# Kernel tuning notes

Hardware: AMD Instinct MI355X
Metric: run time of the kernel (lower is better)

## Reference

```python
import jax, jax.numpy as jnp
import numpy as np

B, F, H, C = 256, 512, 1024, 1000
LN_EPS = 1e-5


def _proj(x, W, b, g, be):
    # AdaptiveAvgPool2d(1) + Flatten + Linear + LayerNorm + GELU(exact)
    p = x.mean(axis=(2, 3))                       # [B, Cin]
    h = p @ W + b                                 # [B, F]
    mu = h.mean(axis=-1, keepdims=True)
    var = h.var(axis=-1, keepdims=True)           # ddof=0, matches torch LayerNorm
    h = (h - mu) / jnp.sqrt(var + LN_EPS) * g + be
    return jax.nn.gelu(h, approximate=False)


def setup_inputs() -> dict:
    key = jax.random.key(0)
    ks = iter(jax.random.split(key, 64))
    def rn(shape, s=1.0):
        return jax.random.normal(next(ks), shape, jnp.float32) * s
    inp = {}
    feats = {"s1": (16, 112), "s2": (24, 56), "s3": (40, 28), "s4": (80, 14), "s5": (160, 7)}
    for n, (c, hw) in feats.items():
        inp[n] = rn((B, c, hw, hw))
    inp["ff"] = rn((B, 960, 7, 7))
    for i, c in enumerate([16, 24, 40, 80, 160], start=1):
        inp[f"Wp{i}"] = rn((c, F), 0.02)
        inp[f"bp{i}"] = jnp.zeros((F,), jnp.float32)
        inp[f"g{i}"] = jnp.ones((F,), jnp.float32)
        inp[f"be{i}"] = jnp.zeros((F,), jnp.float32)
    inp["Wg1"] = rn((960, H), 0.02); inp["bg1"] = jnp.zeros((H,), jnp.float32)
    inp["Wg2"] = rn((H, H // 2), 0.02); inp["bg2"] = jnp.zeros((H // 2,), jnp.float32)
    inp["Wg3"] = rn((H // 2, 5), 0.02); inp["bg3"] = jnp.zeros((5,), jnp.float32)
    inp["Wc1"] = rn((F, H), 0.02); inp["bc1"] = jnp.zeros((H,), jnp.float32)
    inp["Wc2"] = rn((H, H // 2), 0.02); inp["bc2"] = jnp.zeros((H // 2,), jnp.float32)
    inp["Wc3"] = rn((H // 2, C), 0.02); inp["bc3"] = jnp.zeros((C,), jnp.float32)
    return inp


def reference(s1, s2, s3, s4, s5, ff,
              Wp1, bp1, g1, be1, Wp2, bp2, g2, be2, Wp3, bp3, g3, be3,
              Wp4, bp4, g4, be4, Wp5, bp5, g5, be5,
              Wg1, bg1, Wg2, bg2, Wg3, bg3,
              Wc1, bc1, Wc2, bc2, Wc3, bc3):
    # gate on pooled final backbone features (dropout inactive at eval)
    gate_in = ff.mean(axis=(2, 3))                         # [B, 960]
    h = jax.nn.relu(gate_in @ Wg1 + bg1)
    h = jax.nn.relu(h @ Wg2 + bg2)
    gate_logits = h @ Wg3 + bg3                            # [B, 5]

    # per-stage projections -> [B, 5, F]
    stack = jnp.stack([
        _proj(s1, Wp1, bp1, g1, be1),
        _proj(s2, Wp2, bp2, g2, be2),
        _proj(s3, Wp3, bp3, g3, be3),
        _proj(s4, Wp4, bp4, g4, be4),
        _proj(s5, Wp5, bp5, g5, be5),
    ], axis=1)

    topv, topi = jax.lax.top_k(gate_logits, 2)             # [B, 2]
    w = jax.nn.softmax(topv, axis=1)                       # softmax over top-k logits
    sel = jnp.take_along_axis(stack, topi[:, :, None], axis=1)  # [B, 2, F]
    mixture = (sel * w[:, :, None]).sum(axis=1)            # [B, F]

    h = jax.nn.relu(mixture @ Wc1 + bc1)
    h = jax.nn.relu(h @ Wc2 + bc2)
    logits = h @ Wc3 + bc3                                 # [B, C]
    return logits, gate_logits, topi, w
```

## Files before the change

kernel.cpp:

```cpp
#include <hip/hip_runtime.h>
#include <math.h>


struct PoolAll {
    const float* src[4];
    float*       dst[4];
    int n4[4];
    int cum[4];
    float inv[4];
    const float* s5;
    const float* ff;
    float*       dst5;
    float*       dstf;
    int nbb;
    int rows5;
};

__global__ __launch_bounds__(256) void pool_all_kernel(PoolAll S) {
    __shared__ float lds[64 * 49];
    if ((int)blockIdx.x < S.nbb) {
        int gid  = blockIdx.x * 256 + threadIdx.x;
        int wave = gid >> 6;
        int lane = gid & 63;
        if (wave >= S.cum[3]) return;
        int s = 0;
        #pragma unroll
        for (int i = 0; i < 3; ++i) if (wave >= S.cum[i]) s = i + 1;
        int row = wave - (s == 0 ? 0 : S.cum[s - 1]);
        const int n4 = S.n4[s];
        const float4* p4 = (const float4*)(S.src[s]) + (size_t)row * n4;
        float a0 = 0.f, a1 = 0.f, a2 = 0.f, a3 = 0.f;
        float a4 = 0.f, a5 = 0.f, a6 = 0.f, a7 = 0.f;
        int k = lane;
        for (; k + 448 < n4; k += 512) {
            float4 v0 = p4[k];       float4 v1 = p4[k + 64];
            float4 v2 = p4[k + 128]; float4 v3 = p4[k + 192];
            float4 v4 = p4[k + 256]; float4 v5 = p4[k + 320];
            float4 v6 = p4[k + 384]; float4 v7 = p4[k + 448];
            a0 += (v0.x + v0.y) + (v0.z + v0.w);
            a1 += (v1.x + v1.y) + (v1.z + v1.w);
            a2 += (v2.x + v2.y) + (v2.z + v2.w);
            a3 += (v3.x + v3.y) + (v3.z + v3.w);
            a4 += (v4.x + v4.y) + (v4.z + v4.w);
            a5 += (v5.x + v5.y) + (v5.z + v5.w);
            a6 += (v6.x + v6.y) + (v6.z + v6.w);
            a7 += (v7.x + v7.y) + (v7.z + v7.w);
        }
        for (; k + 192 < n4; k += 256) {
            float4 v0 = p4[k];       float4 v1 = p4[k + 64];
            float4 v2 = p4[k + 128]; float4 v3 = p4[k + 192];
            a0 += (v0.x + v0.y) + (v0.z + v0.w);
            a1 += (v1.x + v1.y) + (v1.z + v1.w);
            a2 += (v2.x + v2.y) + (v2.z + v2.w);
            a3 += (v3.x + v3.y) + (v3.z + v3.w);
        }
        for (; k < n4; k += 64) {
            float4 v = p4[k];
            a0 += (v.x + v.y) + (v.z + v.w);
        }
        float acc = ((a0 + a1) + (a2 + a3)) + ((a4 + a5) + (a6 + a7));
        #pragma unroll
        for (int off = 32; off > 0; off >>= 1) acc += __shfl_down(acc, off, 64);
        if (lane == 0) S.dst[s][row] = acc * S.inv[s];
        return;
    }
    const int tid  = threadIdx.x;
    const int row0 = (blockIdx.x - S.nbb) * 64;
    const float* src;
    float* dst;
    int rbase;
    if (row0 < S.rows5) { src = S.s5; dst = S.dst5; rbase = row0; }
    else                { src = S.ff; dst = S.dstf; rbase = row0 - S.rows5; }
    const float4* p4 = (const float4*)(src + (size_t)rbase * 49);
    float4* l4 = (float4*)lds;
    float4 v0 = p4[tid];
    float4 v1 = p4[tid + 256];
    float4 v2 = p4[tid + 512];
    float4 v3;
    const bool t3 = (tid < 784 - 768);
    if (t3) v3 = p4[tid + 768];
    l4[tid]       = v0;
    l4[tid + 256] = v1;
    l4[tid + 512] = v2;
    if (t3) l4[tid + 768] = v3;
    __syncthreads();
    const int r  = tid >> 2;
    const int c0 = tid & 3;
    float s = 0.f;
    #pragma unroll
    for (int c = c0; c < 49; c += 4) s += lds[r * 49 + c];
    s += __shfl_down(s, 2, 64);
    s += __shfl_down(s, 1, 64);
    if (c0 == 0) dst[rbase + r] = s * (1.f / 49.f);
}

template <int XKS, bool EPIB>
__global__ __launch_bounds__(256) void fc_tile_kernel(const float* __restrict__ X,
        const float* __restrict__ xbias, const float* __restrict__ W,
        float* __restrict__ P, const float* __restrict__ bias,
        int M, int K, int N, int Kc, int ntiles) {
    __shared__ __align__(16) float Xs[16][68];
    __shared__ __align__(16) float Ws[16][68];
    const int tpk = 4 * ntiles;
    int bid = blockIdx.x;
    int ks  = bid / tpk;
    int rem = bid - ks * tpk;
    int mt  = rem / ntiles;
    int nt  = rem - mt * ntiles;
    const int m0 = mt * 64, n0 = nt * 64;
    const int k0 = ks * Kc;
    int k1 = k0 + Kc; if (k1 > K) k1 = K;

    const int tid = threadIdx.x;
    const int tm = tid & 15;
    const int tn = tid >> 4;
    const int xr = tid >> 2, xc = tid & 3;
    const int wr = tid >> 4, wc = tid & 15;
    const int nwc = n0 + wc * 4;
    const size_t MK = (size_t)M * K;
    const size_t xoff0 = (size_t)(m0 + xr) * K;

    float4 acc[4];
    #pragma unroll
    for (int r = 0; r < 4; ++r) acc[r] = make_float4(0.f, 0.f, 0.f, 0.f);

    const int NXV = (XKS > 0) ? XKS : 1;
    float4 xv[NXV];
    float4 wv;

    {
        const size_t xo = xoff0 + k0 + xc * 4;
        #pragma unroll
        for (int ss = 0; ss < NXV; ++ss)
            xv[ss] = *(const float4*)(X + (size_t)ss * MK + xo);
        if (nwc + 3 < N) {
            wv = *(const float4*)(W + (size_t)(k0 + wr) * N + nwc);
        } else {
            wv.x = (nwc + 0 < N) ? W[(size_t)(k0 + wr) * N + nwc + 0] : 0.f;
            wv.y = (nwc + 1 < N) ? W[(size_t)(k0 + wr) * N + nwc + 1] : 0.f;
            wv.z = (nwc + 2 < N) ? W[(size_t)(k0 + wr) * N + nwc + 2] : 0.f;
            wv.w = (nwc + 3 < N) ? W[(size_t)(k0 + wr) * N + nwc + 3] : 0.f;
        }
    }

    for (int kt = k0; kt < k1; kt += 16) {
        __syncthreads();
        float4 xs = xv[0];
        if (XKS > 0) {
            #pragma unroll
            for (int ss = 1; ss < NXV; ++ss) {
                xs.x += xv[ss].x; xs.y += xv[ss].y;
                xs.z += xv[ss].z; xs.w += xv[ss].w;
            }
            float4 xb = *(const float4*)(xbias + kt + xc * 4);
            xs.x = fmaxf(xs.x + xb.x, 0.f);
            xs.y = fmaxf(xs.y + xb.y, 0.f);
            xs.z = fmaxf(xs.z + xb.z, 0.f);
            xs.w = fmaxf(xs.w + xb.w, 0.f);
        }
        Xs[xc * 4 + 0][xr] = xs.x;
        Xs[xc * 4 + 1][xr] = xs.y;
        Xs[xc * 4 + 2][xr] = xs.z;
        Xs[xc * 4 + 3][xr] = xs.w;
        *(float4*)&Ws[wr][wc * 4] = wv;
        __syncthreads();
        if (kt + 16 < k1) {
            const size_t xo = xoff0 + kt + 16 + xc * 4;
            #pragma unroll
            for (int ss = 0; ss < NXV; ++ss)
                xv[ss] = *(const float4*)(X + (size_t)ss * MK + xo);
            if (nwc + 3 < N) {
                wv = *(const float4*)(W + (size_t)(kt + 16 + wr) * N + nwc);
            } else {
                wv.x = (nwc + 0 < N) ? W[(size_t)(kt + 16 + wr) * N + nwc + 0] : 0.f;
                wv.y = (nwc + 1 < N) ? W[(size_t)(kt + 16 + wr) * N + nwc + 1] : 0.f;
                wv.z = (nwc + 2 < N) ? W[(size_t)(kt + 16 + wr) * N + nwc + 2] : 0.f;
                wv.w = (nwc + 3 < N) ? W[(size_t)(kt + 16 + wr) * N + nwc + 3] : 0.f;
            }
        }
        #pragma unroll
        for (int kk = 0; kk < 16; ++kk) {
            float4 xr4 = *(const float4*)&Xs[kk][tm * 4];
            float4 wr4 = *(const float4*)&Ws[kk][tn * 4];
            acc[0].x += xr4.x * wr4.x; acc[0].y += xr4.x * wr4.y;
            acc[0].z += xr4.x * wr4.z; acc[0].w += xr4.x * wr4.w;
            acc[1].x += xr4.y * wr4.x; acc[1].y += xr4.y * wr4.y;
            acc[1].z += xr4.y * wr4.z; acc[1].w += xr4.y * wr4.w;
            acc[2].x += xr4.z * wr4.x; acc[2].y += xr4.z * wr4.y;
            acc[2].z += xr4.z * wr4.z; acc[2].w += xr4.z * wr4.w;
            acc[3].x += xr4.w * wr4.x; acc[3].y += xr4.w * wr4.y;
            acc[3].z += xr4.w * wr4.z; acc[3].w += xr4.w * wr4.w;
        }
    }
    const int nbase = n0 + tn * 4;
    #pragma unroll
    for (int r = 0; r < 4; ++r) {
        int row = m0 + tm * 4 + r;
        float* pp = P + ((size_t)ks * M + row) * N + nbase;
        float4 v = acc[r];
        if (EPIB && nbase + 3 < N) {
            float4 bb = *(const float4*)(bias + nbase);
            v.x += bb.x; v.y += bb.y; v.z += bb.z; v.w += bb.w;
        }
        if (nbase + 3 < N) {
            *(float4*)pp = v;
        } else {
            float vv[4] = { v.x, v.y, v.z, v.w };
            for (int c = 0; c < 4; ++c)
                if (nbase + c < N) pp[c] = vv[c] + (EPIB ? bias[nbase + c] : 0.f);
        }
    }
}

struct ProjParams {
    const float* W[5];
    const float* bp[5];
    const float* g[5];
    const float* be[5];
    int K[5];
    int poff[5];
};

__global__ __launch_bounds__(256) void proj_gemm_kernel(ProjParams P,
        const float* __restrict__ pools, float* __restrict__ proj_out) {
    __shared__ __align__(16) float Xs[8][68];
    __shared__ __align__(16) float Ws[8][68];
    const int st = blockIdx.y;
    const int K  = P.K[st];
    const float* X = pools + P.poff[st];
    const float* W = P.W[st];
    const int N = 512;
    int bid = blockIdx.x;
    int mt  = bid >> 3;
    int nt  = bid & 7;
    const int m0 = mt * 64, n0 = nt * 64;

    const int tid = threadIdx.x;
    const int tm = tid & 15;
    const int tn = tid >> 4;
    const int xa = tid >> 3, xb = tid & 7;
    const int wc = tid & 63, wb = tid >> 6;
    const int nw = n0 + wc;

    float4 acc[4];
    #pragma unroll
    for (int r = 0; r < 4; ++r) acc[r] = make_float4(0.f, 0.f, 0.f, 0.f);

    float x0, x1, w0v, w1v;
    x0  = X[(size_t)(m0 + xa) * K + xb];
    x1  = X[(size_t)(m0 + xa + 32) * K + xb];
    w0v = W[(size_t)wb * N + nw];
    w1v = W[(size_t)(wb + 4) * N + nw];

    for (int kt = 0; kt < K; kt += 8) {
        __syncthreads();
        Xs[xb][xa] = x0; Xs[xb][xa + 32] = x1;
        Ws[wb][wc] = w0v; Ws[wb + 4][wc] = w1v;
        __syncthreads();
        if (kt + 8 < K) {
            x0  = X[(size_t)(m0 + xa) * K + kt + 8 + xb];
            x1  = X[(size_t)(m0 + xa + 32) * K + kt + 8 + xb];
            w0v = W[(size_t)(kt + 8 + wb) * N + nw];
            w1v = W[(size_t)(kt + 8 + wb + 4) * N + nw];
        }
        #pragma unroll
        for (int kk = 0; kk < 8; ++kk) {
            float4 xr = *(const float4*)&Xs[kk][tm * 4];
            float4 wr = *(const float4*)&Ws[kk][tn * 4];
            acc[0].x += xr.x * wr.x; acc[0].y += xr.x * wr.y;
            acc[0].z += xr.x * wr.z; acc[0].w += xr.x * wr.w;
            acc[1].x += xr.y * wr.x; acc[1].y += xr.y * wr.y;
            acc[1].z += xr.y * wr.z; acc[1].w += xr.y * wr.w;
            acc[2].x += xr.z * wr.x; acc[2].y += xr.z * wr.y;
            acc[2].z += xr.z * wr.z; acc[2].w += xr.z * wr.w;
            acc[3].x += xr.w * wr.x; acc[3].y += xr.w * wr.y;
            acc[3].z += xr.w * wr.z; acc[3].w += xr.w * wr.w;
        }
    }
    const int nbase = n0 + tn * 4;
    float4 bb = *(const float4*)(P.bp[st] + nbase);
    float* op = proj_out + (size_t)st * 131072 + (size_t)(m0 + tm * 4) * N + nbase;
    #pragma unroll
    for (int r = 0; r < 4; ++r) {
        float4 v = acc[r];
        v.x += bb.x; v.y += bb.y; v.z += bb.z; v.w += bb.w;
        *(float4*)(op + (size_t)r * N) = v;
    }
}

__global__ __launch_bounds__(256) void fc3_top2_kernel(const float* __restrict__ Xp,
        const float* __restrict__ xbias, const float* __restrict__ W,
        const float* __restrict__ bias, int* __restrict__ topi,
        float* __restrict__ wsm, float* __restrict__ out_gl,
        float* __restrict__ out_topi, float* __restrict__ out_w, int K) {
    const int b    = blockIdx.x;
    const int tid  = threadIdx.x;
    const int lane = tid & 63;
    const int wv   = tid >> 6;
    __shared__ float red[4][5];
    const size_t MK = (size_t)256 * K;
    float acc[5] = {0.f, 0.f, 0.f, 0.f, 0.f};
    for (int k = tid; k < K; k += 256) {
        float v = 0.f;
        #pragma unroll
        for (int s = 0; s < 16; ++s) v += Xp[(size_t)s * MK + (size_t)b * K + k];
        float xv = fmaxf(v + xbias[k], 0.f);
        const float* wr = W + (size_t)k * 5;
        acc[0] += xv * wr[0]; acc[1] += xv * wr[1]; acc[2] += xv * wr[2];
        acc[3] += xv * wr[3]; acc[4] += xv * wr[4];
    }
    #pragma unroll
    for (int off = 32; off > 0; off >>= 1) {
        #pragma unroll
        for (int j = 0; j < 5; ++j) acc[j] += __shfl_down(acc[j], off, 64);
    }
    if (lane == 0) {
        #pragma unroll
        for (int j = 0; j < 5; ++j) red[wv][j] = acc[j];
    }
    __syncthreads();
    if (tid == 0) {
        float v[5];
        #pragma unroll
        for (int j = 0; j < 5; ++j)
            v[j] = ((red[0][j] + red[1][j]) + (red[2][j] + red[3][j])) + bias[j];
        int i0 = 0;
        #pragma unroll
        for (int i = 1; i < 5; ++i) if (v[i] > v[i0]) i0 = i;
        int i1 = -1;
        #pragma unroll
        for (int i = 0; i < 5; ++i) {
            if (i == i0) continue;
            if (i1 < 0 || v[i] > v[i1]) i1 = i;
        }
        float e1 = __expf(v[i1] - v[i0]);
        float inv = 1.f / (1.f + e1);
        float w0 = inv, w1 = e1 * inv;
        topi[b * 2] = i0; topi[b * 2 + 1] = i1;
        wsm[b * 2] = w0;  wsm[b * 2 + 1] = w1;
        #pragma unroll
        for (int j = 0; j < 5; ++j) out_gl[b * 5 + j] = v[j];
        out_topi[b * 2]     = (float)i0;
        out_topi[b * 2 + 1] = (float)i1;
        out_w[b * 2]     = w0;
        out_w[b * 2 + 1] = w1;
    }
}

__global__ __launch_bounds__(512) void mixln_kernel(ProjParams P,
        const float* __restrict__ proj_out, const int* __restrict__ topi,
        const float* __restrict__ wsm, float* __restrict__ mix) {
    const int b = blockIdx.x;
    const int f = threadIdx.x;
    __shared__ float redS[8], redQ[8];
    __shared__ float s_mu, s_rstd;

    float acc = 0.f;
    for (int j = 0; j < 2; ++j) {
        __syncthreads();
        const int st = topi[b * 2 + j];
        float h = proj_out[(size_t)st * 131072 + (size_t)b * 512 + f];

        float s = h, q = h * h;
        #pragma unroll
        for (int off = 32; off > 0; off >>= 1) {
            s += __shfl_down(s, off, 64);
            q += __shfl_down(q, off, 64);
        }
        const int lane = threadIdx.x & 63, wid = threadIdx.x >> 6;
        if (lane == 0) { redS[wid] = s; redQ[wid] = q; }
        __syncthreads();
        if (threadIdx.x == 0) {
            float ts = 0.f, tq = 0.f;
            #pragma unroll
            for (int i = 0; i < 8; ++i) { ts += redS[i]; tq += redQ[i]; }
            float mu  = ts * (1.f / 512.f);
            float var = tq * (1.f / 512.f) - mu * mu;
            s_mu   = mu;
            s_rstd = rsqrtf(var + 1e-5f);
        }
        __syncthreads();

        float x  = (h - s_mu) * s_rstd * P.g[st][f] + P.be[st][f];
        float ge = 0.5f * x * (1.f + erff(x * 0.70710678118654752f));
        acc += wsm[b * 2 + j] * ge;
    }
    mix[(size_t)b * 512 + f] = acc;
}

extern "C" void kernel_launch(void* const* d_in, const int* in_sizes, int n_in,
                              void* d_out, int out_size, void* d_ws, size_t ws_size,
                              hipStream_t stream) {
    const int B = 256, F = 512, H = 1024, C = 1000;

    const float* s1 = (const float*)d_in[0];
    const float* s2 = (const float*)d_in[1];
    const float* s3 = (const float*)d_in[2];
    const float* s4 = (const float*)d_in[3];
    const float* s5 = (const float*)d_in[4];
    const float* ff = (const float*)d_in[5];
    const float *Wp[5], *bp[5], *g[5], *be[5];
    for (int i = 0; i < 5; ++i) {
        Wp[i] = (const float*)d_in[6 + 4 * i];
        bp[i] = (const float*)d_in[7 + 4 * i];
        g[i]  = (const float*)d_in[8 + 4 * i];
        be[i] = (const float*)d_in[9 + 4 * i];
    }
    const float* Wg1 = (const float*)d_in[26]; const float* bg1 = (const float*)d_in[27];
    const float* Wg2 = (const float*)d_in[28]; const float* bg2 = (const float*)d_in[29];
    const float* Wg3 = (const float*)d_in[30]; const float* bg3 = (const float*)d_in[31];
    const float* Wc1 = (const float*)d_in[32]; const float* bc1 = (const float*)d_in[33];
    const float* Wc2 = (const float*)d_in[34]; const float* bc2 = (const float*)d_in[35];
    const float* Wc3 = (const float*)d_in[36]; const float* bc3 = (const float*)d_in[37];

    float* ws = (float*)d_ws;
    const int Ks[5]   = {16, 24, 40, 80, 160};
    const int poff[5] = {0, 4096, 10240, 20480, 40960};
    float* pools    = ws;
    float* gate_in  = ws + 81920;
    float* wsm      = ws + 327680;
    int*   topi     = (int*)(ws + 328192);
    float* mix      = ws + 328704;
    float* proj_out = ws + 459776;
    float* slabA    = ws + 1115136;
    float* slabB    = ws + 3212288;

    float* out      = (float*)d_out;
    float* out_gl   = out + 256000;
    float* out_topi = out + 257280;
    float* out_w    = out + 257792;

    {
        PoolAll S;
        const float* srcs[4] = { s1, s2, s3, s4 };
        const int rls[4]  = { 112 * 112, 56 * 56, 28 * 28, 14 * 14 };
        const int rows[4] = { B * 16, B * 24, B * 40, B * 80 };
        int cum = 0;
        for (int i = 0; i < 4; ++i) {
            S.src[i] = srcs[i]; S.dst[i] = pools + poff[i]; S.n4[i] = rls[i] / 4;
            cum += rows[i]; S.cum[i] = cum; S.inv[i] = 1.f / rls[i];
        }
        S.nbb   = (cum * 64) / 256;
        S.s5    = s5; S.ff = ff;
        S.dst5  = pools + poff[4]; S.dstf = gate_in;
        S.rows5 = B * 160;
        int small_blocks = (S.rows5 + B * 960) / 64;
        pool_all_kernel<<<S.nbb + small_blocks, 256, 0, stream>>>(S);
    }

    fc_tile_kernel<0, false><<<8 * 4 * 16, 256, 0, stream>>>(
        gate_in, nullptr, Wg1, slabA, nullptr, B, 960, H, 128, 16);
    fc_tile_kernel<8, false><<<16 * 4 * 8, 256, 0, stream>>>(
        slabA, bg1, Wg2, slabB, nullptr, B, H, H / 2, 64, 8);
    fc3_top2_kernel<<<B, 256, 0, stream>>>(slabB, bg2, Wg3, bg3, topi, wsm,
                                           out_gl, out_topi, out_w, H / 2);

    ProjParams P;
    for (int i = 0; i < 5; ++i) {
        P.W[i] = Wp[i]; P.bp[i] = bp[i]; P.g[i] = g[i]; P.be[i] = be[i];
        P.K[i] = Ks[i]; P.poff[i] = poff[i];
    }
    proj_gemm_kernel<<<dim3(32, 5), 256, 0, stream>>>(P, pools, proj_out);
    mixln_kernel<<<B, 512, 0, stream>>>(P, proj_out, topi, wsm, mix);

    fc_tile_kernel<0, false><<<8 * 4 * 16, 256, 0, stream>>>(
        mix, nullptr, Wc1, slabA, nullptr, B, F, H, 64, 16);
    fc_tile_kernel<8, false><<<16 * 4 * 8, 256, 0, stream>>>(
        slabA, bc1, Wc2, slabB, nullptr, B, H, H / 2, 64, 8);
    fc_tile_kernel<16, true><<<1 * 4 * 16, 256, 0, stream>>>(
        slabB, bc2, Wc3, out, bc3, B, H / 2, C, 512, 16);
}
```

Before: 604.6 us.

## Reduce split-K partials in-kernel via last-block atomic counter; merge fc3 with proj

```diff
diff --git a/kernel.cpp b/kernel.cpp
--- a/kernel.cpp
+++ b/kernel.cpp
@@ -94,22 +94,25 @@
     if (c0 == 0) dst[rbase + r] = s * (1.f / 49.f);
 }
 
-template <int XKS, bool EPIB>
-__global__ __launch_bounds__(256) void fc_tile_kernel(const float* __restrict__ X,
-        const float* __restrict__ xbias, const float* __restrict__ W,
-        float* __restrict__ P, const float* __restrict__ bias,
-        int M, int K, int N, int Kc, int ntiles) {
+__global__ __launch_bounds__(256) void fc_tile_red_kernel(
+        const float* __restrict__ X, const float* __restrict__ W,
+        const float* __restrict__ bias, float* __restrict__ Y,
+        float* __restrict__ Pt, int* __restrict__ cnt,
+        int M, int K, int N, int Kc, int ntiles, int do_relu) {
     __shared__ __align__(16) float Xs[16][68];
     __shared__ __align__(16) float Ws[16][68];
+    __shared__ int s_old;
     const int tpk = 4 * ntiles;
-    int bid = blockIdx.x;
-    int ks  = bid / tpk;
-    int rem = bid - ks * tpk;
-    int mt  = rem / ntiles;
-    int nt  = rem - mt * ntiles;
+    const int bid = blockIdx.x;
+    const int ks  = bid / tpk;
+    const int rem = bid - ks * tpk;
+    const int mt  = rem / ntiles;
+    const int nt  = rem - mt * ntiles;
     const int m0 = mt * 64, n0 = nt * 64;
     const int k0 = ks * Kc;
     int k1 = k0 + Kc; if (k1 > K) k1 = K;
+    const int KS = (K + Kc - 1) / Kc;
+    const int MN = M * N;
 
     const int tid = threadIdx.x;
     const int tm = tid & 15;
@@ -117,58 +120,32 @@
     const int xr = tid >> 2, xc = tid & 3;
     const int wr = tid >> 4, wc = tid & 15;
     const int nwc = n0 + wc * 4;
-    const size_t MK = (size_t)M * K;
-    const size_t xoff0 = (size_t)(m0 + xr) * K;
 
     float4 acc[4];
     #pragma unroll
     for (int r = 0; r < 4; ++r) acc[r] = make_float4(0.f, 0.f, 0.f, 0.f);
 
-    const int NXV = (XKS > 0) ? XKS : 1;
-    float4 xv[NXV];
-    float4 wv;
-
-    {
-        const size_t xo = xoff0 + k0 + xc * 4;
-        #pragma unroll
-        for (int ss = 0; ss < NXV; ++ss)
-            xv[ss] = *(const float4*)(X + (size_t)ss * MK + xo);
-        if (nwc + 3 < N) {
-            wv = *(const float4*)(W + (size_t)(k0 + wr) * N + nwc);
-        } else {
-            wv.x = (nwc + 0 < N) ? W[(size_t)(k0 + wr) * N + nwc + 0] : 0.f;
-            wv.y = (nwc + 1 < N) ? W[(size_t)(k0 + wr) * N + nwc + 1] : 0.f;
-            wv.z = (nwc + 2 < N) ? W[(size_t)(k0 + wr) * N + nwc + 2] : 0.f;
-            wv.w = (nwc + 3 < N) ? W[(size_t)(k0 + wr) * N + nwc + 3] : 0.f;
-        }
+    float4 xv, wv;
+    xv = *(const float4*)(X + (size_t)(m0 + xr) * K + k0 + xc * 4);
+    if (nwc + 3 < N) {
+        wv = *(const float4*)(W + (size_t)(k0 + wr) * N + nwc);
+    } else {
+        wv.x = (nwc + 0 < N) ? W[(size_t)(k0 + wr) * N + nwc + 0] : 0.f;
+        wv.y = (nwc + 1 < N) ? W[(size_t)(k0 + wr) * N + nwc + 1] : 0.f;
+        wv.z = (nwc + 2 < N) ? W[(size_t)(k0 + wr) * N + nwc + 2] : 0.f;
+        wv.w = (nwc + 3 < N) ? W[(size_t)(k0 + wr) * N + nwc + 3] : 0.f;
     }
 
     for (int kt = k0; kt < k1; kt += 16) {
         __syncthreads();
-        float4 xs = xv[0];
-        if (XKS > 0) {
-            #pragma unroll
-            for (int ss = 1; ss < NXV; ++ss) {
-                xs.x += xv[ss].x; xs.y += xv[ss].y;
-                xs.z += xv[ss].z; xs.w += xv[ss].w;
-            }
-            float4 xb = *(const float4*)(xbias + kt + xc * 4);
-            xs.x = fmaxf(xs.x + xb.x, 0.f);
-            xs.y = fmaxf(xs.y + xb.y, 0.f);
-            xs.z = fmaxf(xs.z + xb.z, 0.f);
-            xs.w = fmaxf(xs.w + xb.w, 0.f);
-        }
-        Xs[xc * 4 + 0][xr] = xs.x;
-        Xs[xc * 4 + 1][xr] = xs.y;
-        Xs[xc * 4 + 2][xr] = xs.z;
-        Xs[xc * 4 + 3][xr] = xs.w;
+        Xs[xc * 4 + 0][xr] = xv.x;
+        Xs[xc * 4 + 1][xr] = xv.y;
+        Xs[xc * 4 + 2][xr] = xv.z;
+        Xs[xc * 4 + 3][xr] = xv.w;
         *(float4*)&Ws[wr][wc * 4] = wv;
         __syncthreads();
         if (kt + 16 < k1) {
-            const size_t xo = xoff0 + kt + 16 + xc * 4;
-            #pragma unroll
-            for (int ss = 0; ss < NXV; ++ss)
-                xv[ss] = *(const float4*)(X + (size_t)ss * MK + xo);
+            xv = *(const float4*)(X + (size_t)(m0 + xr) * K + kt + 16 + xc * 4);
             if (nwc + 3 < N) {
                 wv = *(const float4*)(W + (size_t)(kt + 16 + wr) * N + nwc);
             } else {
@@ -192,22 +169,55 @@
             acc[3].z += xr4.w * wr4.z; acc[3].w += xr4.w * wr4.w;
         }
     }
+
     const int nbase = n0 + tn * 4;
     #pragma unroll
     for (int r = 0; r < 4; ++r) {
         int row = m0 + tm * 4 + r;
-        float* pp = P + ((size_t)ks * M + row) * N + nbase;
-        float4 v = acc[r];
-        if (EPIB && nbase + 3 < N) {
+        float* pp = Pt + (size_t)ks * MN + (size_t)row * N + nbase;
+        if (nbase + 3 < N) {
+            *(float4*)pp = acc[r];
+        } else {
+            float vv[4] = { acc[r].x, acc[r].y, acc[r].z, acc[r].w };
+            for (int c = 0; c < 4; ++c) if (nbase + c < N) pp[c] = vv[c];
+        }
+    }
+
+    __threadfence();
+    __syncthreads();
+    if (tid == 0) s_old = atomicAdd(&cnt[rem], 1);
+    __syncthreads();
+    if (s_old != KS - 1) return;
+    __threadfence();
+
+    #pragma unroll
+    for (int r = 0; r < 4; ++r) {
+        int row = m0 + tm * 4 + r;
+        const float* pp = Pt + (size_t)row * N + nbase;
+        if (nbase + 3 < N) {
+            float4 a = *(const float4*)pp;
+            for (int s = 1; s < KS; ++s) {
+                float4 b = *(const float4*)(pp + (size_t)s * MN);
+                a.x += b.x; a.y += b.y; a.z += b.z; a.w += b.w;
+            }
             float4 bb = *(const float4*)(bias + nbase);
-            v.x += bb.x; v.y += bb.y; v.z += bb.z; v.w += bb.w;
-        }
-        if (nbase + 3 < N) {
-            *(float4*)pp = v;
+            a.x += bb.x; a.y += bb.y; a.z += bb.z; a.w += bb.w;
+            if (do_relu) {
+                a.x = fmaxf(a.x, 0.f); a.y = fmaxf(a.y, 0.f);
+                a.z = fmaxf(a.z, 0.f); a.w = fmaxf(a.w, 0.f);
+            }
+            *(float4*)(Y + (size_t)row * N + nbase) = a;
         } else {
-            float vv[4] = { v.x, v.y, v.z, v.w };
-            for (int c = 0; c < 4; ++c)
-                if (nbase + c < N) pp[c] = vv[c] + (EPIB ? bias[nbase + c] : 0.f);
+            for (int c = 0; c < 4; ++c) {
+                int n = nbase + c;
+                if (n < N) {
+                    float a = pp[c];
+                    for (int s = 1; s < KS; ++s) a += pp[c + (size_t)s * MN];
+                    a += bias[n];
+                    if (do_relu) a = fmaxf(a, 0.f);
+                    Y[(size_t)row * N + n] = a;
+                }
+            }
         }
     }
 }
@@ -221,21 +231,80 @@
     int poff[5];
 };
 
-__global__ __launch_bounds__(256) void proj_gemm_kernel(ProjParams P,
-        const float* __restrict__ pools, float* __restrict__ proj_out) {
+__global__ __launch_bounds__(256) void fc3_proj_kernel(
+        const float* __restrict__ Xg, const float* __restrict__ Wg3,
+        const float* __restrict__ bg3, int* __restrict__ topi,
+        float* __restrict__ wsm, float* __restrict__ out_gl,
+        float* __restrict__ out_topi, float* __restrict__ out_w,
+        ProjParams P, const float* __restrict__ pools,
+        float* __restrict__ proj_out) {
     __shared__ __align__(16) float Xs[8][68];
     __shared__ __align__(16) float Ws[8][68];
-    const int st = blockIdx.y;
+    __shared__ float red[4][5];
+    const int tid = threadIdx.x;
+
+    if (blockIdx.x < 256) {
+        const int b    = blockIdx.x;
+        const int lane = tid & 63;
+        const int wv   = tid >> 6;
+        const float* x = Xg + (size_t)b * 512;
+        float acc[5] = {0.f, 0.f, 0.f, 0.f, 0.f};
+        for (int k = tid; k < 512; k += 256) {
+            float xv = x[k];
+            const float* wr = Wg3 + (size_t)k * 5;
+            acc[0] += xv * wr[0]; acc[1] += xv * wr[1]; acc[2] += xv * wr[2];
+            acc[3] += xv * wr[3]; acc[4] += xv * wr[4];
+        }
+        #pragma unroll
+        for (int off = 32; off > 0; off >>= 1) {
+            #pragma unroll
+            for (int j = 0; j < 5; ++j) acc[j] += __shfl_down(acc[j], off, 64);
+        }
+        if (lane == 0) {
+            #pragma unroll
+            for (int j = 0; j < 5; ++j) red[wv][j] = acc[j];
+        }
+        __syncthreads();
+        if (tid == 0) {
+            float v[5];
+            #pragma unroll
+            for (int j = 0; j < 5; ++j)
+                v[j] = ((red[0][j] + red[1][j]) + (red[2][j] + red[3][j])) + bg3[j];
+            int i0 = 0;
+            #pragma unroll
+            for (int i = 1; i < 5; ++i) if (v[i] > v[i0]) i0 = i;
+            int i1 = -1;
+            #pragma unroll
+            for (int i = 0; i < 5; ++i) {
+                if (i == i0) continue;
+                if (i1 < 0 || v[i] > v[i1]) i1 = i;
+            }
+            float e1 = __expf(v[i1] - v[i0]);
+            float inv = 1.f / (1.f + e1);
+            float w0 = inv, w1 = e1 * inv;
+            topi[b * 2] = i0; topi[b * 2 + 1] = i1;
+            wsm[b * 2] = w0;  wsm[b * 2 + 1] = w1;
+            #pragma unroll
+            for (int j = 0; j < 5; ++j) out_gl[b * 5 + j] = v[j];
+            out_topi[b * 2]     = (float)i0;
+            out_topi[b * 2 + 1] = (float)i1;
+            out_w[b * 2]     = w0;
+            out_w[b * 2 + 1] = w1;
+        }
+        return;
+    }
+
+    const int task = blockIdx.x - 256;
+    const int st  = task >> 5;
+    const int bid = task & 31;
     const int K  = P.K[st];
     const float* X = pools + P.poff[st];
     const float* W = P.W[st];
     const int N = 512;
-    int bid = blockIdx.x;
     int mt  = bid >> 3;
     int nt  = bid & 7;
     const int m0 = mt * 64, n0 = nt * 64;
 
-    const int tid = threadIdx.x;
     const int tm = tid & 15;
     const int tn = tid >> 4;
     const int xa = tid >> 3, xb = tid & 7;
@@ -288,65 +357,6 @@
     }
 }
 
-__global__ __launch_bounds__(256) void fc3_top2_kernel(const float* __restrict__ Xp,
-        const float* __restrict__ xbias, const float* __restrict__ W,
-        const float* __restrict__ bias, int* __restrict__ topi,
-        float* __restrict__ wsm, float* __restrict__ out_gl,
-        float* __restrict__ out_topi, float* __restrict__ out_w, int K) {
-    const int b    = blockIdx.x;
-    const int tid  = threadIdx.x;
-    const int lane = tid & 63;
-    const int wv   = tid >> 6;
-    __shared__ float red[4][5];
-    const size_t MK = (size_t)256 * K;
-    float acc[5] = {0.f, 0.f, 0.f, 0.f, 0.f};
-    for (int k = tid; k < K; k += 256) {
-        float v = 0.f;
-        #pragma unroll
-        for (int s = 0; s < 16; ++s) v += Xp[(size_t)s * MK + (size_t)b * K + k];
-        float xv = fmaxf(v + xbias[k], 0.f);
-        const float* wr = W + (size_t)k * 5;
-        acc[0] += xv * wr[0]; acc[1] += xv * wr[1]; acc[2] += xv * wr[2];
-        acc[3] += xv * wr[3]; acc[4] += xv * wr[4];
-    }
-    #pragma unroll
-    for (int off = 32; off > 0; off >>= 1) {
-        #pragma unroll
-        for (int j = 0; j < 5; ++j) acc[j] += __shfl_down(acc[j], off, 64);
-    }
-    if (lane == 0) {
-        #pragma unroll
-        for (int j = 0; j < 5; ++j) red[wv][j] = acc[j];
-    }
-    __syncthreads();
-    if (tid == 0) {
-        float v[5];
-        #pragma unroll
-        for (int j = 0; j < 5; ++j)
-            v[j] = ((red[0][j] + red[1][j]) + (red[2][j] + red[3][j])) + bias[j];
-        int i0 = 0;
-        #pragma unroll
-        for (int i = 1; i < 5; ++i) if (v[i] > v[i0]) i0 = i;
-        int i1 = -1;
-        #pragma unroll
-        for (int i = 0; i < 5; ++i) {
-            if (i == i0) continue;
-            if (i1 < 0 || v[i] > v[i1]) i1 = i;
-        }
-        float e1 = __expf(v[i1] - v[i0]);
-        float inv = 1.f / (1.f + e1);
-        float w0 = inv, w1 = e1 * inv;
-        topi[b * 2] = i0; topi[b * 2 + 1] = i1;
-        wsm[b * 2] = w0;  wsm[b * 2 + 1] = w1;
-        #pragma unroll
-        for (int j = 0; j < 5; ++j) out_gl[b * 5 + j] = v[j];
-        out_topi[b * 2]     = (float)i0;
-        out_topi[b * 2 + 1] = (float)i1;
-        out_w[b * 2]     = w0;
-        out_w[b * 2 + 1] = w1;
-    }
-}
-
 __global__ __launch_bounds__(512) void mixln_kernel(ProjParams P,
         const float* __restrict__ proj_out, const int* __restrict__ topi,
         const float* __restrict__ wsm, float* __restrict__ mix) {
@@ -391,7 +401,7 @@
 extern "C" void kernel_launch(void* const* d_in, const int* in_sizes, int n_in,
                               void* d_out, int out_size, void* d_ws, size_t ws_size,
                               hipStream_t stream) {
-    const int B = 256, F = 512, H = 1024, C = 1000;
+    const int B = 256;
 
     const float* s1 = (const float*)d_in[0];
     const float* s2 = (const float*)d_in[1];
@@ -418,17 +428,23 @@
     const int poff[5] = {0, 4096, 10240, 20480, 40960};
     float* pools    = ws;
     float* gate_in  = ws + 81920;
-    float* wsm      = ws + 327680;
-    int*   topi     = (int*)(ws + 328192);
-    float* mix      = ws + 328704;
-    float* proj_out = ws + 459776;
-    float* slabA    = ws + 1115136;
-    float* slabB    = ws + 3212288;
+    float* g1h      = ws + 327680;
+    float* g2h      = ws + 589824;
+    float* wsm      = ws + 720896;
+    int*   topi     = (int*)(ws + 721408);
+    float* mix      = ws + 721920;
+    float* proj_out = ws + 852992;
+    float* c1h      = ws + 1508352;
+    float* c2h      = ws + 1770496;
+    int*   cnt      = (int*)(ws + 1901568);
+    float* slab     = ws + 1901824;
 
     float* out      = (float*)d_out;
     float* out_gl   = out + 256000;
     float* out_topi = out + 257280;
     float* out_w    = out + 257792;
+
+    hipMemsetAsync(cnt, 0, 256 * sizeof(int), stream);
 
     {
         PoolAll S;
@@ -448,25 +464,25 @@
         pool_all_kernel<<<S.nbb + small_blocks, 256, 0, stream>>>(S);
     }
 
-    fc_tile_kernel<0, false><<<8 * 4 * 16, 256, 0, stream>>>(
-        gate_in, nullptr, Wg1, slabA, nullptr, B, 960, H, 128, 16);
-    fc_tile_kernel<8, false><<<16 * 4 * 8, 256, 0, stream>>>(
-        slabA, bg1, Wg2, slabB, nullptr, B, H, H / 2, 64, 8);
-    fc3_top2_kernel<<<B, 256, 0, stream>>>(slabB, bg2, Wg3, bg3, topi, wsm,
-                                           out_gl, out_topi, out_w, H / 2);
+    fc_tile_red_kernel<<<8 * 4 * 16, 256, 0, stream>>>(
+        gate_in, Wg1, bg1, g1h, slab, cnt + 0, 256, 960, 1024, 128, 16, 1);
+    fc_tile_red_kernel<<<16 * 4 * 8, 256, 0, stream>>>(
+        g1h, Wg2, bg2, g2h, slab, cnt + 64, 256, 1024, 512, 64, 8, 1);
 
     ProjParams P;
     for (int i = 0; i < 5; ++i) {
         P.W[i] = Wp[i]; P.bp[i] = bp[i]; P.g[i] = g[i]; P.be[i] = be[i];
         P.K[i] = Ks[i]; P.poff[i] = poff[i];
     }
-    proj_gemm_kernel<<<dim3(32, 5), 256, 0, stream>>>(P, pools, proj_out);
+    fc3_proj_kernel<<<416, 256, 0, stream>>>(g2h, Wg3, bg3, topi, wsm,
+                                             out_gl, out_topi, out_w,
+                                             P, pools, proj_out);
     mixln_kernel<<<B, 512, 0, stream>>>(P, proj_out, topi, wsm, mix);
 
-    fc_tile_kernel<0, false><<<8 * 4 * 16, 256, 0, stream>>>(
-        mix, nullptr, Wc1, slabA, nullptr, B, F, H, 64, 16);
-    fc_tile_kernel<8, false><<<16 * 4 * 8, 256, 0, stream>>>(
-        slabA, bc1, Wc2, slabB, nullptr, B, H, H / 2, 64, 8);
-    fc_tile_kernel<16, true><<<1 * 4 * 16, 256, 0, stream>>>(
-        slabB, bc2, Wc3, out, bc3, B, H / 2, C, 512, 16);
+    fc_tile_red_kernel<<<8 * 4 * 16, 256, 0, stream>>>(
+        mix, Wc1, bc1, c1h, slab, cnt + 96, 256, 512, 1024, 64, 16, 1);
+    fc_tile_red_kernel<<<16 * 4 * 8, 256, 0, stream>>>(
+        c1h, Wc2, bc2, c2h, slab, cnt + 160, 256, 1024, 512, 64, 8, 1);
+    fc_tile_red_kernel<<<8 * 4 * 16, 256, 0, stream>>>(
+        c2h, Wc3, bc3, out, slab, cnt + 192, 256, 512, 1000, 64, 16, 0);
 }
```

New measurement: 917.0 us. 51.7% more time.
